# Optimization experiments

Hardware: AMD Instinct MI355X
Metric: run time of the kernel (lower is better)

The kernel has to match this reference:

```python
import jax, jax.numpy as jnp
import numpy as np

B, C, N, M, H = 2, 512, 2048, 2048, 8
HD = C // H
SCALE = HD ** -0.5


def setup_inputs() -> dict:
    key = jax.random.key(0)
    ks = jax.random.split(key, 8)
    x = jax.random.normal(ks[0], (B, C, N), dtype=jnp.float32)
    y = jax.random.normal(ks[1], (B, C, M), dtype=jnp.float32)
    # linear weights stored as [in, out] so out = in @ W (equivalent to torch Linear)
    Wq = jax.random.normal(ks[2], (C, C), dtype=jnp.float32) * (C ** -0.5)
    Wkv = jax.random.normal(ks[3], (C, 2 * C), dtype=jnp.float32) * (C ** -0.5)
    # depthwise Conv1d, kernel_size=1, groups=C -> per-channel scale + bias
    lw = jax.random.normal(ks[4], (C,), dtype=jnp.float32)
    lb = jax.random.normal(ks[5], (C,), dtype=jnp.float32) * 0.01
    Wp = jax.random.normal(ks[6], (C, C), dtype=jnp.float32) * (C ** -0.5)
    bp = jax.random.normal(ks[7], (C,), dtype=jnp.float32) * 0.01
    return {"x": x, "y": y, "Wq": Wq, "Wkv": Wkv, "lw": lw, "lb": lb, "Wp": Wp, "bp": bp}


def reference(x, y, Wq, Wkv, lw, lb, Wp, bp):
    # x: [B,C,N], y: [B,C,M]
    q = (x.transpose(0, 2, 1) @ Wq).reshape(B, N, H, HD).transpose(0, 2, 1, 3)  # [B,H,N,HD]
    kv = (y.transpose(0, 2, 1) @ Wkv).reshape(B, M, H, HD, 2).transpose(0, 2, 1, 3, 4)
    k, v = kv[..., 0], kv[..., 1]  # [B,H,M,HD]
    attn = jax.nn.softmax(jnp.einsum('bhnd,bhmd->bhnm', q, k) * SCALE, axis=-1)
    # depthwise conv1d (ksize=1) on v laid out as [B,C,M]; channel c = h*HD + d
    lw2 = lw.reshape(H, HD)[None, :, None, :]
    lb2 = lb.reshape(H, HD)[None, :, None, :]
    v = v + v * lw2 + lb2
    out = jnp.einsum('bhnm,bhmd->bhnd', attn, v).transpose(0, 2, 1, 3).reshape(B, N, C)
    out = (out @ Wp + bp).transpose(0, 2, 1)  # [B,C,N]
    return out
```

## Files before the change

### kernel.cpp

```cpp
#include <hip/hip_runtime.h>

#define Bb 2
#define Cc 512
#define Nn 2048
#define Mm 2048
#define Hh 8
#define HD 64
#define QSCALE 0.18033688011112042f

typedef unsigned short u16;
typedef unsigned int u32;
typedef __bf16 bf16x8 __attribute__((ext_vector_type(8)));
typedef float f32x16 __attribute__((ext_vector_type(16)));

union V4 {
    uint4 u;
    bf16x8 b;
};

__device__ __forceinline__ u16 f2bfu(float f) {
    unsigned int b = __float_as_uint(f);
    unsigned int r = (b + 0x7fffu + ((b >> 16) & 1u)) >> 16;
    return (u16)r;
}
__device__ __forceinline__ u32 pkbf(float lo, float hi_) {
    return __builtin_amdgcn_perm(__float_as_uint(hi_) + 0x8000u,
                                 __float_as_uint(lo) + 0x8000u, 0x07060302u);
}

__global__ __launch_bounds__(256) void transpose_all(
    const float* __restrict__ x, const float* __restrict__ y, const float* __restrict__ Wq,
    const float* __restrict__ Wkv, const float* __restrict__ Wp, u16* __restrict__ xT,
    u16* __restrict__ yT, u16* __restrict__ WqT, u16* __restrict__ WkvT,
    u16* __restrict__ WpT) {
    __shared__ float tile[32][33];
    const int z = blockIdx.z;
    const float* in;
    u16* out;
    int S, sx = blockIdx.x;
    size_t base = 0;
    const int R = 512;
    if (z < 4) {
        in = (z < 2) ? x : y;
        out = (z < 2) ? xT : yT;
        S = 2048;
        base = (size_t)(z & 1) * R * S;
    } else {
        if (sx < 16) {
            in = Wq; out = WqT; S = 512;
        } else if (sx < 48) {
            in = Wkv; out = WkvT; S = 1024; sx -= 16;
        } else {
            in = Wp; out = WpT; S = 512; sx -= 48;
        }
    }
    int r0 = blockIdx.y * 32, s0 = sx * 32;
    int tx = threadIdx.x, ty = threadIdx.y;
#pragma unroll
    for (int k = 0; k < 4; k++)
        tile[ty + 8 * k][tx] = in[base + (size_t)(r0 + ty + 8 * k) * S + s0 + tx];
    __syncthreads();
#pragma unroll
    for (int k = 0; k < 4; k++)
        out[base + (size_t)(s0 + ty + 8 * k) * R + r0 + tx] = f2bfu(tile[tx][ty + 8 * k]);
}

__global__ __launch_bounds__(256) void proj_qkv(const u16* __restrict__ xT,
                                                const u16* __restrict__ yT,
                                                const u16* __restrict__ WqT,
                                                const u16* __restrict__ WkvT,
                                                const float* __restrict__ lw,
                                                const float* __restrict__ lb,
                                                u16* __restrict__ qb, u16* __restrict__ kb,
                                                u16* __restrict__ vtb) {
    __shared__ alignas(16) u16 As[2][128 * 64];
    __shared__ alignas(16) u16 Bs[2][64 * 64];
    const int t = threadIdx.x;
    const int lane = t & 63, w = t >> 6;
    const int r = lane & 31, hi = lane >> 5;
    const bool isQ = (blockIdx.x < 8);
    const int c0 = (isQ ? blockIdx.x : blockIdx.x - 8) * 64;
    const int r0 = blockIdx.y * 128;
    const int wr = (w & 1) * 64, wc = (w >> 1) * 32;
    const u16* A = isQ ? xT : yT;
    const u16* Bt = isQ ? WqT : WkvT;

    const int sra = t >> 3, ska = t & 7;
    const int swa = ((ska ^ (sra & 7)) << 3);
    const u16* Ag = A + (size_t)(r0 + sra) * 512 + ska * 8;
    const u16* Bg = Bt + (size_t)(c0 + sra) * 512 + ska * 8;

    {
#pragma unroll
        for (int i = 0; i < 4; i++)
            *(uint4*)&As[0][(sra + 32 * i) * 64 + swa] = *(const uint4*)(Ag + (size_t)i * 32 * 512);
#pragma unroll
        for (int i = 0; i < 2; i++)
            *(uint4*)&Bs[0][(sra + 32 * i) * 64 + swa] = *(const uint4*)(Bg + (size_t)i * 32 * 512);
    }
    __syncthreads();

    f32x16 acc[2];
#pragma unroll
    for (int rs = 0; rs < 2; rs++)
#pragma unroll
        for (int e = 0; e < 16; e++) acc[rs][e] = 0.f;

    const int ra0 = wr + r, ra1 = wr + 32 + r, rb = wc + r;

    for (int kk = 0; kk < 8; kk++) {
        const int cur = kk & 1;
        uint4 pa[4], pb[2];
        const bool more = (kk < 7);
        if (more) {
            const size_t ko = (size_t)(kk + 1) * 64;
#pragma unroll
            for (int i = 0; i < 4; i++) pa[i] = *(const uint4*)(Ag + (size_t)i * 32 * 512 + ko);
#pragma unroll
            for (int i = 0; i < 2; i++) pb[i] = *(const uint4*)(Bg + (size_t)i * 32 * 512 + ko);
        }
        V4 af[2][4], bf[4];
#pragma unroll
        for (int ks = 0; ks < 4; ks++) {
            const int c = 2 * ks + hi;
            bf[ks].u = *(const uint4*)&Bs[cur][rb * 64 + ((c ^ (rb & 7)) << 3)];
            af[0][ks].u = *(const uint4*)&As[cur][ra0 * 64 + ((c ^ (ra0 & 7)) << 3)];
            af[1][ks].u = *(const uint4*)&As[cur][ra1 * 64 + ((c ^ (ra1 & 7)) << 3)];
        }
#pragma unroll
        for (int ks = 0; ks < 4; ks++) {
            acc[0] = __builtin_amdgcn_mfma_f32_32x32x16_bf16(af[0][ks].b, bf[ks].b, acc[0], 0, 0, 0);
            acc[1] = __builtin_amdgcn_mfma_f32_32x32x16_bf16(af[1][ks].b, bf[ks].b, acc[1], 0, 0, 0);
        }
        if (more) {
            const int nxt = cur ^ 1;
#pragma unroll
            for (int i = 0; i < 4; i++) *(uint4*)&As[nxt][(sra + 32 * i) * 64 + swa] = pa[i];
#pragma unroll
            for (int i = 0; i < 2; i++) *(uint4*)&Bs[nxt][(sra + 32 * i) * 64 + swa] = pb[i];
        }
        __syncthreads();
    }

    const int cg = c0 + wc + r;
    if (isQ) {
#pragma unroll
        for (int rs = 0; rs < 2; rs++)
#pragma unroll
            for (int e = 0; e < 16; e++) {
                int m = r0 + wr + rs * 32 + 4 * hi + (e & 3) + 8 * (e >> 2);
                qb[(size_t)m * 512 + cg] = f2bfu(acc[rs][e] * QSCALE);
            }
    } else {
        const int hd = cg >> 1, s = cg & 1, h = hd >> 6, d = hd & 63;
        const int bq = r0 >> 11;
        const int bh = bq * 8 + h;
        const int mb = (r0 & 2047) + wr + 4 * hi;
        if (s == 0) {
            u16* kbase = kb + ((size_t)bh * 2048) * 64 + d;
#pragma unroll
            for (int rs = 0; rs < 2; rs++)
#pragma unroll
                for (int e = 0; e < 16; e++) {
                    int m = mb + rs * 32 + (e & 3) + 8 * (e >> 2);
                    kbase[(size_t)m * 64] = f2bfu(acc[rs][e]);
                }
        } else {
            const float sw = 1.0f + lw[hd], sb = lb[hd];
            u16* vbase = vtb + ((size_t)bh * 64 + d) * 2048;
#pragma unroll
            for (int rs = 0; rs < 2; rs++)
#pragma unroll
                for (int eg = 0; eg < 4; eg++) {
                    int m = mb + rs * 32 + 8 * eg;
                    float v0 = acc[rs][4 * eg + 0] * sw + sb;
                    float v1 = acc[rs][4 * eg + 1] * sw + sb;
                    float v2 = acc[rs][4 * eg + 2] * sw + sb;
                    float v3 = acc[rs][4 * eg + 3] * sw + sb;
                    uint2 pk;
                    pk.x = pkbf(v0, v1);
                    pk.y = pkbf(v2, v3);
                    *(uint2*)(vbase + m) = pk;
                }
        }
    }
}

__global__ __launch_bounds__(256, 4) void flash_attn(const u16* __restrict__ q,
                                                     const u16* __restrict__ kk,
                                                     const u16* __restrict__ vt,
                                                     float* __restrict__ po,
                                                     float* __restrict__ ls) {
    __shared__ alignas(16) u16 Ks[2][64 * 64];
    __shared__ alignas(16) u16 Vs[2][64 * 64];
    const int t = threadIdx.x;
    const int lane = t & 63, w = t >> 6;
    const int r = lane & 31, hi = lane >> 5;
    const int nt = blockIdx.x & 15, sp = blockIdx.x >> 4;
    const int h = blockIdx.y, b = blockIdx.z;
    const int bh = b * Hh + h;
    const int nw = nt * 128 + 32 * w + r;
    const int MT0 = sp * 8, MT1 = MT0 + 8;

    V4 qf[4];
    {
        const u16* qrow = q + ((size_t)(b * Nn + nw)) * Cc + h * HD + hi * 8;
#pragma unroll
        for (int ks = 0; ks < 4; ks++) qf[ks].u = *(const uint4*)(qrow + ks * 16);
    }

    const u16* kbase = kk + ((size_t)bh) * Mm * HD;
    const u16* vbase = vt + ((size_t)bh) * HD * Mm;

    const int cr0 = t >> 3, cc0 = t & 7;
    const int cr1 = cr0 + 32, cc1 = cc0;
    const int swa0 = cr0 * 64 + ((cc0 ^ (cr0 & 7)) << 3);
    const int swa1 = cr1 * 64 + ((cc1 ^ (cr1 & 7)) << 3);

    {
        int m00 = MT0 * 64;
        uint4 a0 = *(const uint4*)(kbase + (size_t)(m00 + cr0) * HD + cc0 * 8);
        uint4 a1 = *(const uint4*)(kbase + (size_t)(m00 + cr1) * HD + cc1 * 8);
        uint4 b0 = *(const uint4*)(vbase + (size_t)cr0 * Mm + m00 + cc0 * 8);
        uint4 b1 = *(const uint4*)(vbase + (size_t)cr1 * Mm + m00 + cc1 * 8);
        *(uint4*)&Ks[0][swa0] = a0;
        *(uint4*)&Ks[0][swa1] = a1;
        *(uint4*)&Vs[0][swa0] = b0;
        *(uint4*)&Vs[0][swa1] = b1;
    }
    __syncthreads();

    f32x16 oa0, oa1;
#pragma unroll
    for (int e = 0; e < 16; e++) {
        oa0[e] = 0.f;
        oa1[e] = 0.f;
    }
    float lsum = 0.f;

    for (int mt = MT0; mt < MT1; mt++) {
        const int cur = mt & 1;
        uint4 nk0, nk1, nv0, nv1;
        const bool more = (mt + 1 < MT1);
        if (more) {
            int m0 = (mt + 1) * 64;
            nk0 = *(const uint4*)(kbase + (size_t)(m0 + cr0) * HD + cc0 * 8);
            nk1 = *(const uint4*)(kbase + (size_t)(m0 + cr1) * HD + cc1 * 8);
            nv0 = *(const uint4*)(vbase + (size_t)cr0 * Mm + m0 + cc0 * 8);
            nv1 = *(const uint4*)(vbase + (size_t)cr1 * Mm + m0 + cc1 * 8);
        }
        f32x16 sa[2];
#pragma unroll
        for (int s = 0; s < 2; s++) {
#pragma unroll
            for (int e = 0; e < 16; e++) sa[s][e] = 0.f;
#pragma unroll
            for (int ks = 0; ks < 4; ks++) {
                V4 af;
                af.u = *(const uint4*)&Ks[cur][(32 * s + r) * 64 +
                                               (((2 * ks + hi) ^ (r & 7)) << 3)];
                sa[s] = __builtin_amdgcn_mfma_f32_32x32x16_bf16(af.b, qf[ks].b, sa[s], 0, 0, 0);
            }
        }
#pragma unroll
        for (int s = 0; s < 2; s++) {
            u32 p[8];
#pragma unroll
            for (int qq = 0; qq < 8; qq++) {
                float e0 = __builtin_amdgcn_exp2f(sa[s][2 * qq]);
                float e1 = __builtin_amdgcn_exp2f(sa[s][2 * qq + 1]);
                lsum += e0 + e1;
                p[qq] = pkbf(e0, e1);
            }
            u32 xr0 = __shfl_xor(hi ? p[0] : p[2], 32);
            u32 xr1 = __shfl_xor(hi ? p[1] : p[3], 32);
            u32 xr2 = __shfl_xor(hi ? p[4] : p[6], 32);
            u32 xr3 = __shfl_xor(hi ? p[5] : p[7], 32);
#pragma unroll
            for (int kl = 0; kl < 2; kl++) {
                V4 pf;
                if (kl == 0) {
                    pf.u.x = hi ? xr0 : p[0];
                    pf.u.y = hi ? xr1 : p[1];
                    pf.u.z = hi ? p[2] : xr0;
                    pf.u.w = hi ? p[3] : xr1;
                } else {
                    pf.u.x = hi ? xr2 : p[4];
                    pf.u.y = hi ? xr3 : p[5];
                    pf.u.z = hi ? p[6] : xr2;
                    pf.u.w = hi ? p[7] : xr3;
                }
                const int c = 4 * s + 2 * kl + hi;
                V4 vf0, vf1;
                vf0.u = *(const uint4*)&Vs[cur][r * 64 + ((c ^ (r & 7)) << 3)];
                vf1.u = *(const uint4*)&Vs[cur][(32 + r) * 64 + ((c ^ (r & 7)) << 3)];
                oa0 = __builtin_amdgcn_mfma_f32_32x32x16_bf16(vf0.b, pf.b, oa0, 0, 0, 0);
                oa1 = __builtin_amdgcn_mfma_f32_32x32x16_bf16(vf1.b, pf.b, oa1, 0, 0, 0);
            }
        }
        if (more) {
            const int nxt = cur ^ 1;
            *(uint4*)&Ks[nxt][swa0] = nk0;
            *(uint4*)&Ks[nxt][swa1] = nk1;
            *(uint4*)&Vs[nxt][swa0] = nv0;
            *(uint4*)&Vs[nxt][swa1] = nv1;
        }
        __syncthreads();
    }

    lsum += __shfl_xor(lsum, 32);
    float* pob = po + (((size_t)sp * 16 + bh) * 64) * 2048 + nw;
#pragma unroll
    for (int e = 0; e < 16; e++) {
        int d0 = (e & 3) + 8 * (e >> 2) + 4 * hi;
        pob[(size_t)d0 * 2048] = oa0[e];
        pob[(size_t)(d0 + 32) * 2048] = oa1[e];
    }
    if (hi == 0) ls[((size_t)sp * 16 + bh) * 2048 + nw] = lsum;
}

__global__ __launch_bounds__(256) void combine_o(const float* __restrict__ po,
                                                 const float* __restrict__ ls,
                                                 u16* __restrict__ o) {
    __shared__ u16 tile[64][72];
    const int t = threadIdx.x;
    const int n0 = blockIdx.x * 64, bh = blockIdx.y;
    const int n = n0 + (t & 63), dg = t >> 6;
    float linv;
    {
        float s = 0.f;
#pragma unroll
        for (int sp = 0; sp < 4; sp++) s += ls[((size_t)sp * 16 + bh) * 2048 + n];
        linv = 1.0f / s;
    }
#pragma unroll
    for (int i = 0; i < 16; i++) {
        int d = dg * 16 + i;
        float acc = 0.f;
#pragma unroll
        for (int sp = 0; sp < 4; sp++)
            acc += po[(((size_t)sp * 16 + bh) * 64 + d) * 2048 + n];
        tile[t & 63][d] = f2bfu(acc * linv);
    }
    __syncthreads();
    const int nr = t >> 2, dq = (t & 3) * 16;
    const int b = bh >> 3, h = bh & 7;
    u16* orow = o + ((size_t)(b * Nn + n0 + nr)) * Cc + h * 64 + dq;
    *(uint4*)(orow + 0) = *(const uint4*)&tile[nr][dq];
    *(uint4*)(orow + 8) = *(const uint4*)&tile[nr][dq + 8];
}

__global__ __launch_bounds__(256) void gemm_out(const u16* __restrict__ Wt,
                                                const u16* __restrict__ Ob,
                                                float* __restrict__ out,
                                                const float* __restrict__ bias) {
    __shared__ alignas(16) u16 Ws[2][64 * 64];
    __shared__ alignas(16) u16 Os[2][128 * 64];
    const int t = threadIdx.x;
    const int lane = t & 63, w = t >> 6;
    const int r = lane & 31, hi = lane >> 5;
    const int c0 = blockIdx.x * 64, n0 = blockIdx.y * 128;
    const int cb = (w & 1) * 32, nb = (w >> 1) * 32;

    const int sra = t >> 3, ska = t & 7;
    const int swa = ((ska ^ (sra & 7)) << 3);
    const u16* Wg = Wt + (size_t)(c0 + sra) * 512 + ska * 8;
    const u16* Og = Ob + (size_t)(n0 + sra) * 512 + ska * 8;

    {
#pragma unroll
        for (int i = 0; i < 2; i++)
            *(uint4*)&Ws[0][(sra + 32 * i) * 64 + swa] = *(const uint4*)(Wg + (size_t)i * 32 * 512);
#pragma unroll
        for (int i = 0; i < 4; i++)
            *(uint4*)&Os[0][(sra + 32 * i) * 64 + swa] = *(const uint4*)(Og + (size_t)i * 32 * 512);
    }
    __syncthreads();

    f32x16 acc[2];
#pragma unroll
    for (int ns = 0; ns < 2; ns++)
#pragma unroll
        for (int e = 0; e < 16; e++) acc[ns][e] = 0.f;

    const int rw = cb + r, ro0 = nb + r, ro1 = nb + 64 + r;

    for (int kk = 0; kk < 8; kk++) {
        const int cur = kk & 1;
        uint4 pw[2], po_[4];
        const bool more = (kk < 7);
        if (more) {
            const size_t ko = (size_t)(kk + 1) * 64;
#pragma unroll
            for (int i = 0; i < 2; i++) pw[i] = *(const uint4*)(Wg + (size_t)i * 32 * 512 + ko);
#pragma unroll
            for (int i = 0; i < 4; i++) po_[i] = *(const uint4*)(Og + (size_t)i * 32 * 512 + ko);
        }
        V4 wf[4], of[2][4];
#pragma unroll
        for (int ks = 0; ks < 4; ks++) {
            const int c = 2 * ks + hi;
            wf[ks].u = *(const uint4*)&Ws[cur][rw * 64 + ((c ^ (rw & 7)) << 3)];
            of[0][ks].u = *(const uint4*)&Os[cur][ro0 * 64 + ((c ^ (ro0 & 7)) << 3)];
            of[1][ks].u = *(const uint4*)&Os[cur][ro1 * 64 + ((c ^ (ro1 & 7)) << 3)];
        }
#pragma unroll
        for (int ks = 0; ks < 4; ks++) {
            acc[0] = __builtin_amdgcn_mfma_f32_32x32x16_bf16(wf[ks].b, of[0][ks].b, acc[0], 0, 0, 0);
            acc[1] = __builtin_amdgcn_mfma_f32_32x32x16_bf16(wf[ks].b, of[1][ks].b, acc[1], 0, 0, 0);
        }
        if (more) {
            const int nxt = cur ^ 1;
#pragma unroll
            for (int i = 0; i < 2; i++) *(uint4*)&Ws[nxt][(sra + 32 * i) * 64 + swa] = pw[i];
#pragma unroll
            for (int i = 0; i < 4; i++) *(uint4*)&Os[nxt][(sra + 32 * i) * 64 + swa] = po_[i];
        }
        __syncthreads();
    }

#pragma unroll
    for (int e = 0; e < 16; e++) {
        const int c_r = c0 + cb + 4 * hi + (e & 3) + 8 * (e >> 2);
        const float bv = bias[c_r];
#pragma unroll
        for (int ns = 0; ns < 2; ns++) {
            const int rg = n0 + nb + ns * 64 + r;
            const int b = rg >> 11, n = rg & 2047;
            out[((size_t)b * 512 + c_r) * 2048 + n] = acc[ns][e] + bv;
        }
    }
}

static const size_t OFF_XT = 0;
static const size_t OFF_YT = 4194304;
static const size_t OFF_WQT = 8388608;
static const size_t OFF_WKVT = 8912896;
static const size_t OFF_WPT = 9961472;
static const size_t OFF_Q = 10485760;
static const size_t OFF_K = 23068672;
static const size_t OFF_VT = 27262976;
static const size_t OFF_O = 31457280;
static const size_t OFF_PO = 35651584;
static const size_t OFF_LS = 69206016;

extern "C" void kernel_launch(void* const* d_in, const int* in_sizes, int n_in,
                              void* d_out, int out_size, void* d_ws, size_t ws_size,
                              hipStream_t stream) {
    const float* x = (const float*)d_in[0];
    const float* y = (const float*)d_in[1];
    const float* Wq = (const float*)d_in[2];
    const float* Wkv = (const float*)d_in[3];
    const float* lw = (const float*)d_in[4];
    const float* lb = (const float*)d_in[5];
    const float* Wp = (const float*)d_in[6];
    const float* bp = (const float*)d_in[7];

    char* ws = (char*)d_ws;
    u16* xT = (u16*)(ws + OFF_XT);
    u16* yT = (u16*)(ws + OFF_YT);
    u16* WqT = (u16*)(ws + OFF_WQT);
    u16* WkvT = (u16*)(ws + OFF_WKVT);
    u16* WpT = (u16*)(ws + OFF_WPT);
    u16* qb = (u16*)(ws + OFF_Q);
    u16* kb = (u16*)(ws + OFF_K);
    u16* vtb = (u16*)(ws + OFF_VT);
    u16* ob = (u16*)(ws + OFF_O);
    float* po = (float*)(ws + OFF_PO);
    float* lsw = (float*)(ws + OFF_LS);

    dim3 tb(32, 8, 1);
    transpose_all<<<dim3(64, 16, 5), tb, 0, stream>>>(x, y, Wq, Wkv, Wp, xT, yT, WqT, WkvT,
                                                      WpT);
    proj_qkv<<<dim3(24, 32), 256, 0, stream>>>(xT, yT, WqT, WkvT, lw, lb, qb, kb, vtb);
    flash_attn<<<dim3(64, Hh, Bb), 256, 0, stream>>>(qb, kb, vtb, po, lsw);
    combine_o<<<dim3(Nn / 64, Bb * Hh), 256, 0, stream>>>(po, lsw, ob);
    gemm_out<<<dim3(8, 32), 256, 0, stream>>>(WpT, ob, (float*)d_out, bp);
}
```

Before: 142.6 us.

## Load K/V fragments directly from global memory, dropping LDS staging and barriers

The flash attention kernel no longer stages K and V tiles through double-buffered shared memory with __syncthreads. Each wave now reads its MFMA operand fragments straight from global memory through per-lane pointers, relying on L1/L2 to serve the reads shared by the four waves of a block. The launch-bounds occupancy hint also drops from 4 to 3 blocks. This removes LDS traffic and block barriers, but each wave now issues its own global loads for data the whole block shares, and the loads are no longer prefetched a tile ahead.

```diff
diff --git a/kernel.cpp b/kernel.cpp
--- a/kernel.cpp
+++ b/kernel.cpp
@@ -186,13 +186,11 @@
     }
 }
 
-__global__ __launch_bounds__(256, 4) void flash_attn(const u16* __restrict__ q,
+__global__ __launch_bounds__(256, 3) void flash_attn(const u16* __restrict__ q,
                                                      const u16* __restrict__ kk,
                                                      const u16* __restrict__ vt,
                                                      float* __restrict__ po,
                                                      float* __restrict__ ls) {
-    __shared__ alignas(16) u16 Ks[2][64 * 64];
-    __shared__ alignas(16) u16 Vs[2][64 * 64];
     const int t = threadIdx.x;
     const int lane = t & 63, w = t >> 6;
     const int r = lane & 31, hi = lane >> 5;
@@ -200,7 +198,7 @@
     const int h = blockIdx.y, b = blockIdx.z;
     const int bh = b * Hh + h;
     const int nw = nt * 128 + 32 * w + r;
-    const int MT0 = sp * 8, MT1 = MT0 + 8;
+    const int MT0 = sp * 8;
 
     V4 qf[4];
     {
@@ -209,26 +207,9 @@
         for (int ks = 0; ks < 4; ks++) qf[ks].u = *(const uint4*)(qrow + ks * 16);
     }
 
-    const u16* kbase = kk + ((size_t)bh) * Mm * HD;
-    const u16* vbase = vt + ((size_t)bh) * HD * Mm;
-
-    const int cr0 = t >> 3, cc0 = t & 7;
-    const int cr1 = cr0 + 32, cc1 = cc0;
-    const int swa0 = cr0 * 64 + ((cc0 ^ (cr0 & 7)) << 3);
-    const int swa1 = cr1 * 64 + ((cc1 ^ (cr1 & 7)) << 3);
-
-    {
-        int m00 = MT0 * 64;
-        uint4 a0 = *(const uint4*)(kbase + (size_t)(m00 + cr0) * HD + cc0 * 8);
-        uint4 a1 = *(const uint4*)(kbase + (size_t)(m00 + cr1) * HD + cc1 * 8);
-        uint4 b0 = *(const uint4*)(vbase + (size_t)cr0 * Mm + m00 + cc0 * 8);
-        uint4 b1 = *(const uint4*)(vbase + (size_t)cr1 * Mm + m00 + cc1 * 8);
-        *(uint4*)&Ks[0][swa0] = a0;
-        *(uint4*)&Ks[0][swa1] = a1;
-        *(uint4*)&Vs[0][swa0] = b0;
-        *(uint4*)&Vs[0][swa1] = b1;
-    }
-    __syncthreads();
+    const u16* kp = kk + ((size_t)bh) * Mm * HD + (size_t)(MT0 * 64 + r) * HD + hi * 8;
+    const u16* vp0 = vt + ((size_t)bh) * HD * Mm + (size_t)r * Mm + MT0 * 64 + hi * 8;
+    const u16* vp1 = vp0 + 32 * Mm;
 
     f32x16 oa0, oa1;
 #pragma unroll
@@ -238,17 +219,7 @@
     }
     float lsum = 0.f;
 
-    for (int mt = MT0; mt < MT1; mt++) {
-        const int cur = mt & 1;
-        uint4 nk0, nk1, nv0, nv1;
-        const bool more = (mt + 1 < MT1);
-        if (more) {
-            int m0 = (mt + 1) * 64;
-            nk0 = *(const uint4*)(kbase + (size_t)(m0 + cr0) * HD + cc0 * 8);
-            nk1 = *(const uint4*)(kbase + (size_t)(m0 + cr1) * HD + cc1 * 8);
-            nv0 = *(const uint4*)(vbase + (size_t)cr0 * Mm + m0 + cc0 * 8);
-            nv1 = *(const uint4*)(vbase + (size_t)cr1 * Mm + m0 + cc1 * 8);
-        }
+    for (int mt = 0; mt < 8; mt++) {
         f32x16 sa[2];
 #pragma unroll
         for (int s = 0; s < 2; s++) {
@@ -257,8 +228,7 @@
 #pragma unroll
             for (int ks = 0; ks < 4; ks++) {
                 V4 af;
-                af.u = *(const uint4*)&Ks[cur][(32 * s + r) * 64 +
-                                               (((2 * ks + hi) ^ (r & 7)) << 3)];
+                af.u = *(const uint4*)(kp + s * 32 * HD + ks * 16);
                 sa[s] = __builtin_amdgcn_mfma_f32_32x32x16_bf16(af.b, qf[ks].b, sa[s], 0, 0, 0);
             }
         }
@@ -290,22 +260,16 @@
                     pf.u.z = hi ? p[6] : xr2;
                     pf.u.w = hi ? p[7] : xr3;
                 }
-                const int c = 4 * s + 2 * kl + hi;
                 V4 vf0, vf1;
-                vf0.u = *(const uint4*)&Vs[cur][r * 64 + ((c ^ (r & 7)) << 3)];
-                vf1.u = *(const uint4*)&Vs[cur][(32 + r) * 64 + ((c ^ (r & 7)) << 3)];
+                vf0.u = *(const uint4*)(vp0 + (4 * s + 2 * kl) * 8);
+                vf1.u = *(const uint4*)(vp1 + (4 * s + 2 * kl) * 8);
                 oa0 = __builtin_amdgcn_mfma_f32_32x32x16_bf16(vf0.b, pf.b, oa0, 0, 0, 0);
                 oa1 = __builtin_amdgcn_mfma_f32_32x32x16_bf16(vf1.b, pf.b, oa1, 0, 0, 0);
             }
         }
-        if (more) {
-            const int nxt = cur ^ 1;
-            *(uint4*)&Ks[nxt][swa0] = nk0;
-            *(uint4*)&Ks[nxt][swa1] = nk1;
-            *(uint4*)&Vs[nxt][swa0] = nv0;
-            *(uint4*)&Vs[nxt][swa1] = nv1;
-        }
-        __syncthreads();
+        kp += 64 * HD;
+        vp0 += 64;
+        vp1 += 64;
     }
 
     lsum += __shfl_xor(lsum, 32);
```

Measured after the change: 187.4 us. +31.4%, slower.

## Process two query tiles per wave in flash attention to reuse K/V fragments

Applied to the files above, without the earlier changes.

Each wave now handles 64 query rows (two 32-row MFMA tiles) instead of 32, so every K and V fragment loaded from LDS feeds two MFMAs. The block covers 256 queries, and the grid halves to 32 x-blocks. This is meant to cut LDS read traffic and global K/V tile loads per unit of work. In exchange it roughly doubles accumulator registers, lowers the occupancy hint from 4 to 2, and launches half as many blocks (512), which may underfill the GPU.

```diff
diff --git a/kernel.cpp b/kernel.cpp
--- a/kernel.cpp
+++ b/kernel.cpp
@@ -186,7 +186,7 @@
     }
 }
 
-__global__ __launch_bounds__(256, 4) void flash_attn(const u16* __restrict__ q,
+__global__ __launch_bounds__(256, 2) void flash_attn(const u16* __restrict__ q,
                                                      const u16* __restrict__ kk,
                                                      const u16* __restrict__ vt,
                                                      float* __restrict__ po,
@@ -196,17 +196,20 @@
     const int t = threadIdx.x;
     const int lane = t & 63, w = t >> 6;
     const int r = lane & 31, hi = lane >> 5;
-    const int nt = blockIdx.x & 15, sp = blockIdx.x >> 4;
+    const int nt = blockIdx.x & 7, sp = blockIdx.x >> 3;
     const int h = blockIdx.y, b = blockIdx.z;
     const int bh = b * Hh + h;
-    const int nw = nt * 128 + 32 * w + r;
+    const int nw0 = nt * 256 + 64 * w + r;
     const int MT0 = sp * 8, MT1 = MT0 + 8;
 
-    V4 qf[4];
+    V4 qf[2][4];
     {
-        const u16* qrow = q + ((size_t)(b * Nn + nw)) * Cc + h * HD + hi * 8;
-#pragma unroll
-        for (int ks = 0; ks < 4; ks++) qf[ks].u = *(const uint4*)(qrow + ks * 16);
+        const u16* qrow = q + ((size_t)(b * Nn + nw0)) * Cc + h * HD + hi * 8;
+#pragma unroll
+        for (int ks = 0; ks < 4; ks++) {
+            qf[0][ks].u = *(const uint4*)(qrow + ks * 16);
+            qf[1][ks].u = *(const uint4*)(qrow + 32 * Cc + ks * 16);
+        }
     }
 
     const u16* kbase = kk + ((size_t)bh) * Mm * HD;
@@ -230,13 +233,14 @@
     }
     __syncthreads();
 
-    f32x16 oa0, oa1;
-#pragma unroll
-    for (int e = 0; e < 16; e++) {
-        oa0[e] = 0.f;
-        oa1[e] = 0.f;
-    }
-    float lsum = 0.f;
+    f32x16 oa[2][2];
+#pragma unroll
+    for (int v = 0; v < 2; v++)
+#pragma unroll
+        for (int nh = 0; nh < 2; nh++)
+#pragma unroll
+            for (int e = 0; e < 16; e++) oa[v][nh][e] = 0.f;
+    float lsum0 = 0.f, lsum1 = 0.f;
 
     for (int mt = MT0; mt < MT1; mt++) {
         const int cur = mt & 1;
@@ -249,53 +253,71 @@
             nv0 = *(const uint4*)(vbase + (size_t)cr0 * Mm + m0 + cc0 * 8);
             nv1 = *(const uint4*)(vbase + (size_t)cr1 * Mm + m0 + cc1 * 8);
         }
-        f32x16 sa[2];
+        f32x16 sa[2][2];
 #pragma unroll
         for (int s = 0; s < 2; s++) {
 #pragma unroll
-            for (int e = 0; e < 16; e++) sa[s][e] = 0.f;
+            for (int nh = 0; nh < 2; nh++)
+#pragma unroll
+                for (int e = 0; e < 16; e++) sa[s][nh][e] = 0.f;
 #pragma unroll
             for (int ks = 0; ks < 4; ks++) {
                 V4 af;
                 af.u = *(const uint4*)&Ks[cur][(32 * s + r) * 64 +
                                                (((2 * ks + hi) ^ (r & 7)) << 3)];
-                sa[s] = __builtin_amdgcn_mfma_f32_32x32x16_bf16(af.b, qf[ks].b, sa[s], 0, 0, 0);
+                sa[s][0] = __builtin_amdgcn_mfma_f32_32x32x16_bf16(af.b, qf[0][ks].b,
+                                                                   sa[s][0], 0, 0, 0);
+                sa[s][1] = __builtin_amdgcn_mfma_f32_32x32x16_bf16(af.b, qf[1][ks].b,
+                                                                   sa[s][1], 0, 0, 0);
             }
         }
 #pragma unroll
         for (int s = 0; s < 2; s++) {
-            u32 p[8];
+            u32 p[2][8];
 #pragma unroll
             for (int qq = 0; qq < 8; qq++) {
-                float e0 = __builtin_amdgcn_exp2f(sa[s][2 * qq]);
-                float e1 = __builtin_amdgcn_exp2f(sa[s][2 * qq + 1]);
-                lsum += e0 + e1;
-                p[qq] = pkbf(e0, e1);
+                float e0 = __builtin_amdgcn_exp2f(sa[s][0][2 * qq]);
+                float e1 = __builtin_amdgcn_exp2f(sa[s][0][2 * qq + 1]);
+                lsum0 += e0 + e1;
+                p[0][qq] = pkbf(e0, e1);
+                float f0 = __builtin_amdgcn_exp2f(sa[s][1][2 * qq]);
+                float f1 = __builtin_amdgcn_exp2f(sa[s][1][2 * qq + 1]);
+                lsum1 += f0 + f1;
+                p[1][qq] = pkbf(f0, f1);
             }
-            u32 xr0 = __shfl_xor(hi ? p[0] : p[2], 32);
-            u32 xr1 = __shfl_xor(hi ? p[1] : p[3], 32);
-            u32 xr2 = __shfl_xor(hi ? p[4] : p[6], 32);
-            u32 xr3 = __shfl_xor(hi ? p[5] : p[7], 32);
+            u32 xr[2][4];
+#pragma unroll
+            for (int nh = 0; nh < 2; nh++) {
+                xr[nh][0] = __shfl_xor(hi ? p[nh][0] : p[nh][2], 32);
+                xr[nh][1] = __shfl_xor(hi ? p[nh][1] : p[nh][3], 32);
+                xr[nh][2] = __shfl_xor(hi ? p[nh][4] : p[nh][6], 32);
+                xr[nh][3] = __shfl_xor(hi ? p[nh][5] : p[nh][7], 32);
+            }
 #pragma unroll
             for (int kl = 0; kl < 2; kl++) {
-                V4 pf;
-                if (kl == 0) {
-                    pf.u.x = hi ? xr0 : p[0];
-                    pf.u.y = hi ? xr1 : p[1];
-                    pf.u.z = hi ? p[2] : xr0;
-                    pf.u.w = hi ? p[3] : xr1;
-                } else {
-                    pf.u.x = hi ? xr2 : p[4];
-                    pf.u.y = hi ? xr3 : p[5];
-                    pf.u.z = hi ? p[6] : xr2;
-                    pf.u.w = hi ? p[7] : xr3;
+                V4 pf[2];
+#pragma unroll
+                for (int nh = 0; nh < 2; nh++) {
+                    if (kl == 0) {
+                        pf[nh].u.x = hi ? xr[nh][0] : p[nh][0];
+                        pf[nh].u.y = hi ? xr[nh][1] : p[nh][1];
+                        pf[nh].u.z = hi ? p[nh][2] : xr[nh][0];
+                        pf[nh].u.w = hi ? p[nh][3] : xr[nh][1];
+                    } else {
+                        pf[nh].u.x = hi ? xr[nh][2] : p[nh][4];
+                        pf[nh].u.y = hi ? xr[nh][3] : p[nh][5];
+                        pf[nh].u.z = hi ? p[nh][6] : xr[nh][2];
+                        pf[nh].u.w = hi ? p[nh][7] : xr[nh][3];
+                    }
                 }
                 const int c = 4 * s + 2 * kl + hi;
                 V4 vf0, vf1;
                 vf0.u = *(const uint4*)&Vs[cur][r * 64 + ((c ^ (r & 7)) << 3)];
                 vf1.u = *(const uint4*)&Vs[cur][(32 + r) * 64 + ((c ^ (r & 7)) << 3)];
-                oa0 = __builtin_amdgcn_mfma_f32_32x32x16_bf16(vf0.b, pf.b, oa0, 0, 0, 0);
-                oa1 = __builtin_amdgcn_mfma_f32_32x32x16_bf16(vf1.b, pf.b, oa1, 0, 0, 0);
+                oa[0][0] = __builtin_amdgcn_mfma_f32_32x32x16_bf16(vf0.b, pf[0].b, oa[0][0], 0, 0, 0);
+                oa[0][1] = __builtin_amdgcn_mfma_f32_32x32x16_bf16(vf0.b, pf[1].b, oa[0][1], 0, 0, 0);
+                oa[1][0] = __builtin_amdgcn_mfma_f32_32x32x16_bf16(vf1.b, pf[0].b, oa[1][0], 0, 0, 0);
+                oa[1][1] = __builtin_amdgcn_mfma_f32_32x32x16_bf16(vf1.b, pf[1].b, oa[1][1], 0, 0, 0);
             }
         }
         if (more) {
@@ -308,15 +330,21 @@
         __syncthreads();
     }
 
-    lsum += __shfl_xor(lsum, 32);
-    float* pob = po + (((size_t)sp * 16 + bh) * 64) * 2048 + nw;
+    lsum0 += __shfl_xor(lsum0, 32);
+    lsum1 += __shfl_xor(lsum1, 32);
+    float* pob = po + (((size_t)sp * 16 + bh) * 64) * 2048 + nw0;
 #pragma unroll
     for (int e = 0; e < 16; e++) {
         int d0 = (e & 3) + 8 * (e >> 2) + 4 * hi;
-        pob[(size_t)d0 * 2048] = oa0[e];
-        pob[(size_t)(d0 + 32) * 2048] = oa1[e];
-    }
-    if (hi == 0) ls[((size_t)sp * 16 + bh) * 2048 + nw] = lsum;
+        pob[(size_t)d0 * 2048] = oa[0][0][e];
+        pob[(size_t)(d0 + 32) * 2048] = oa[1][0][e];
+        pob[(size_t)d0 * 2048 + 32] = oa[0][1][e];
+        pob[(size_t)(d0 + 32) * 2048 + 32] = oa[1][1][e];
+    }
+    if (hi == 0) {
+        ls[((size_t)sp * 16 + bh) * 2048 + nw0] = lsum0;
+        ls[((size_t)sp * 16 + bh) * 2048 + nw0 + 32] = lsum1;
+    }
 }
 
 __global__ __launch_bounds__(256) void combine_o(const float* __restrict__ po,
@@ -473,7 +501,7 @@
     transpose_all<<<dim3(64, 16, 5), tb, 0, stream>>>(x, y, Wq, Wkv, Wp, xT, yT, WqT, WkvT,
                                                       WpT);
     proj_qkv<<<dim3(24, 32), 256, 0, stream>>>(xT, yT, WqT, WkvT, lw, lb, qb, kb, vtb);
-    flash_attn<<<dim3(64, Hh, Bb), 256, 0, stream>>>(qb, kb, vtb, po, lsw);
+    flash_attn<<<dim3(32, Hh, Bb), 256, 0, stream>>>(qb, kb, vtb, po, lsw);
     combine_o<<<dim3(Nn / 64, Bb * Hh), 256, 0, stream>>>(po, lsw, ob);
     gemm_out<<<dim3(8, 32), 256, 0, stream>>>(WpT, ob, (float*)d_out, bp);
 }
```

Result: faster. 138.0 us (-3.3%).
